# Kernel tuning notes

Measured on AMD Instinct MI355X. Metric: run time of the kernel, lower is better.

Reference implementation:

```python
import jax, jax.numpy as jnp
import numpy as np

HIDDEN_DIM = 2048
NUM_EXPERTS = 64
TOP_K = 2
NUM_TOKENS = 16384


def setup_inputs() -> dict:
    key = jax.random.key(0)
    kx, kw, kb = jax.random.split(key, 3)
    X = jax.random.normal(kx, (NUM_TOKENS, HIDDEN_DIM), dtype=jnp.float32)
    # nn.Linear(hidden_dim, num_experts): weight [num_experts, hidden_dim], bias [num_experts]
    bound = 1.0 / np.sqrt(HIDDEN_DIM)
    W = jax.random.uniform(kw, (NUM_EXPERTS, HIDDEN_DIM), minval=-bound, maxval=bound, dtype=jnp.float32)
    b = jax.random.uniform(kb, (NUM_EXPERTS,), minval=-bound, maxval=bound, dtype=jnp.float32)
    return {"X": X, "W": W, "b": b}


def reference(X, W, b):
    # router_logits = gate(X): [T, E]
    router_logits = jnp.einsum("th,eh->te", X, W) + b
    # softmax in float32 (matches dtype=torch.float)
    routing_probs = jax.nn.softmax(router_logits.astype(jnp.float32), axis=-1)
    # top-k over experts: [T, K]
    router_weights, selected_experts = jax.lax.top_k(routing_probs, TOP_K)
    # renormalize over selected experts (sum cast to X.dtype, result stays fp32 math)
    denom = jnp.sum(router_weights, axis=-1, keepdims=True).astype(X.dtype)
    router_weights = router_weights / denom
    # one-hot expert mask: [T, K, E], int64 like F.one_hot
    expert_mask = jax.nn.one_hot(selected_experts, NUM_EXPERTS, dtype=jnp.int32)
    return (router_logits, router_weights, selected_experts, expert_mask)
```

## Files before the change

kernel.cpp:

```cpp
#include <hip/hip_runtime.h>
#include <math.h>

constexpr int T_TOK = 16384;
constexpr int HDIM  = 2048;
constexpr int NEXP  = 64;
constexpr int TPB   = 64;
constexpr int NWAVE = 8;
constexpr int KPW   = HDIM / NWAVE;
constexpr int KSTEP = 32;
constexpr int NKS   = KPW / KSTEP;

typedef __attribute__((ext_vector_type(8))) short v8s;
typedef __attribute__((ext_vector_type(4))) float v4f;

#define MFMA_BF16 __builtin_amdgcn_mfma_f32_16x16x32_bf16

static __device__ __forceinline__ void split3(float x, unsigned short& h,
                                              unsigned short& m, unsigned short& l)
{
    unsigned u0 = __float_as_uint(x);
    h = (unsigned short)(u0 >> 16);
    float r1 = x - __uint_as_float(u0 & 0xFFFF0000u);
    unsigned u1 = __float_as_uint(r1);
    m = (unsigned short)(u1 >> 16);
    float r2 = r1 - __uint_as_float(u1 & 0xFFFF0000u);
    l = (unsigned short)(__float_as_uint(r2) >> 16);
}

static __device__ __forceinline__ void frag3(const float4& x0, const float4& x1,
                                             v8s& h, v8s& m, v8s& l)
{
    unsigned short sh, sm, sl;
    split3(x0.x, sh, sm, sl); h[0]=(short)sh; m[0]=(short)sm; l[0]=(short)sl;
    split3(x0.y, sh, sm, sl); h[1]=(short)sh; m[1]=(short)sm; l[1]=(short)sl;
    split3(x0.z, sh, sm, sl); h[2]=(short)sh; m[2]=(short)sm; l[2]=(short)sl;
    split3(x0.w, sh, sm, sl); h[3]=(short)sh; m[3]=(short)sm; l[3]=(short)sl;
    split3(x1.x, sh, sm, sl); h[4]=(short)sh; m[4]=(short)sm; l[4]=(short)sl;
    split3(x1.y, sh, sm, sl); h[5]=(short)sh; m[5]=(short)sm; l[5]=(short)sl;
    split3(x1.z, sh, sm, sl); h[6]=(short)sh; m[6]=(short)sm; l[6]=(short)sl;
    split3(x1.w, sh, sm, sl); h[7]=(short)sh; m[7]=(short)sm; l[7]=(short)sl;
}

static __device__ __forceinline__ int swz_e(int tok, int e) {
    return e ^ (((tok >> 2) & 1) << 4);
}

__global__ __launch_bounds__(512, 2)
void moe_router_mfma(const float* __restrict__ X,
                     const float* __restrict__ Wg,
                     const float* __restrict__ Bg,
                     float* __restrict__ out)
{
    __shared__ float red[4][TPB][NEXP];

    const int tid  = threadIdx.x;
    const int lane = tid & 63;
    const int wv   = tid >> 6;
    const int r16  = lane & 15;
    const int q    = lane >> 4;
    const int tok0 = blockIdx.x * TPB;

    const float* pA = X  + (size_t)(tok0 + r16) * HDIM + wv * KPW + q * 8;
    const float* pB = Wg + (size_t)r16 * HDIM + wv * KPW + q * 8;

    v4f acc[4][4];
#pragma unroll
    for (int mt = 0; mt < 4; ++mt)
#pragma unroll
        for (int nt = 0; nt < 4; ++nt)
            acc[mt][nt] = (v4f){0.f, 0.f, 0.f, 0.f};

    float4 a0[4], a1[4], b0[4], b1[4];
#pragma unroll
    for (int mt = 0; mt < 4; ++mt) {
        const float* p = pA + (size_t)mt * 16 * HDIM;
        a0[mt] = *(const float4*)p;
        a1[mt] = *(const float4*)(p + 4);
    }
#pragma unroll
    for (int nt = 0; nt < 4; ++nt) {
        const float* p = pB + (size_t)nt * 16 * HDIM;
        b0[nt] = *(const float4*)p;
        b1[nt] = *(const float4*)(p + 4);
    }

    for (int ks = 0; ks < NKS; ++ks) {
        v8s Ah[4], Am[4], Al[4], Bh[4], Bm[4], Bl[4];
#pragma unroll
        for (int mt = 0; mt < 4; ++mt) frag3(a0[mt], a1[mt], Ah[mt], Am[mt], Al[mt]);
#pragma unroll
        for (int nt = 0; nt < 4; ++nt) frag3(b0[nt], b1[nt], Bh[nt], Bm[nt], Bl[nt]);

        if (ks < NKS - 1) {
            const int off = (ks + 1) * KSTEP;
#pragma unroll
            for (int mt = 0; mt < 4; ++mt) {
                const float* p = pA + (size_t)mt * 16 * HDIM + off;
                a0[mt] = *(const float4*)p;
                a1[mt] = *(const float4*)(p + 4);
            }
#pragma unroll
            for (int nt = 0; nt < 4; ++nt) {
                const float* p = pB + (size_t)nt * 16 * HDIM + off;
                b0[nt] = *(const float4*)p;
                b1[nt] = *(const float4*)(p + 4);
            }
        }

#pragma unroll
        for (int mt = 0; mt < 4; ++mt)
#pragma unroll
            for (int nt = 0; nt < 4; ++nt) {
                v4f a = acc[mt][nt];
                a = MFMA_BF16(Ah[mt], Bh[nt], a, 0, 0, 0);
                a = MFMA_BF16(Ah[mt], Bm[nt], a, 0, 0, 0);
                a = MFMA_BF16(Am[mt], Bh[nt], a, 0, 0, 0);
                a = MFMA_BF16(Ah[mt], Bl[nt], a, 0, 0, 0);
                a = MFMA_BF16(Al[mt], Bh[nt], a, 0, 0, 0);
                a = MFMA_BF16(Am[mt], Bm[nt], a, 0, 0, 0);
                acc[mt][nt] = a;
            }
    }

    if (wv < 4) {
#pragma unroll
        for (int mt = 0; mt < 4; ++mt)
#pragma unroll
            for (int nt = 0; nt < 4; ++nt)
#pragma unroll
                for (int r = 0; r < 4; ++r) {
                    int tok = 16 * mt + q * 4 + r;
                    int e   = 16 * nt + r16;
                    red[wv][tok][swz_e(tok, e)] = acc[mt][nt][r];
                }
    }
    __syncthreads();
    if (wv >= 4) {
#pragma unroll
        for (int mt = 0; mt < 4; ++mt)
#pragma unroll
            for (int nt = 0; nt < 4; ++nt)
#pragma unroll
                for (int r = 0; r < 4; ++r) {
                    int tok = 16 * mt + q * 4 + r;
                    int e   = 16 * nt + r16;
                    red[wv - 4][tok][swz_e(tok, e)] += acc[mt][nt][r];
                }
    }
    __syncthreads();

    if (lane < 8) {
        const int tk = wv * 8 + lane;
        const int t  = tok0 + tk;
        float lg[NEXP];
#pragma unroll
        for (int e = 0; e < NEXP; ++e) {
            int es = swz_e(tk, e);
            lg[e] = ((red[0][tk][es] + red[1][tk][es]) +
                     (red[2][tk][es] + red[3][tk][es])) + Bg[e];
        }
        float* outL = out + (size_t)t * NEXP;
#pragma unroll
        for (int e = 0; e < NEXP; e += 4) {
            float4 v = make_float4(lg[e], lg[e+1], lg[e+2], lg[e+3]);
            *(float4*)(outL + e) = v;
        }
        float mx = lg[0];
#pragma unroll
        for (int e = 1; e < NEXP; ++e) mx = fmaxf(mx, lg[e]);
        float S = 0.f;
#pragma unroll
        for (int e = 0; e < NEXP; ++e) { lg[e] = expf(lg[e] - mx); S += lg[e]; }
#pragma unroll
        for (int e = 0; e < NEXP; ++e) lg[e] = lg[e] / S;

        float v1 = lg[0]; int i1 = 0;
        float v2 = -1.0f; int i2 = 0;
#pragma unroll
        for (int e = 1; e < NEXP; ++e) {
            float rv = lg[e];
            bool g1 = rv > v1;
            bool g2 = rv > v2;
            float nv2 = g1 ? v1 : (g2 ? rv : v2);
            int   ni2 = g1 ? i1 : (g2 ? e  : i2);
            v2 = nv2; i2 = ni2;
            v1 = g1 ? rv : v1;
            i1 = g1 ? e  : i1;
        }
        float den = v1 + v2;
        float w1 = v1 / den, w2 = v2 / den;

        float* outW = out + (size_t)T_TOK * NEXP;
        float* outS = outW + (size_t)T_TOK * 2;
        float* outM = outS + (size_t)T_TOK * 2;
        outW[2*t+0] = w1;        outW[2*t+1] = w2;
        outS[2*t+0] = (float)i1; outS[2*t+1] = (float)i2;

        float* mrow = outM + (size_t)t * 2 * NEXP;
#pragma unroll
        for (int e = 0; e < NEXP; e += 4) {
            float4 a = make_float4(e+0==i1?1.f:0.f, e+1==i1?1.f:0.f,
                                   e+2==i1?1.f:0.f, e+3==i1?1.f:0.f);
            *(float4*)(mrow + e) = a;
            float4 b = make_float4(e+0==i2?1.f:0.f, e+1==i2?1.f:0.f,
                                   e+2==i2?1.f:0.f, e+3==i2?1.f:0.f);
            *(float4*)(mrow + NEXP + e) = b;
        }
    }
}

extern "C" void kernel_launch(void* const* d_in, const int* in_sizes, int n_in,
                              void* d_out, int out_size, void* d_ws, size_t ws_size,
                              hipStream_t stream)
{
    const float* X = (const float*)d_in[0];
    const float* W = (const float*)d_in[1];
    const float* B = (const float*)d_in[2];
    float* out     = (float*)d_out;

    dim3 grid(T_TOK / TPB);
    dim3 block(512);
    hipLaunchKernelGGL(moe_router_mfma, grid, block, 0, stream, X, W, B, out);
}
```

Baseline: 222.3 us.

## Halve tokens per block to double grid size and raise occupancy

Cuts the token tile per block from 64 to 32, which doubles the grid and raises the launch-bounds occupancy hint from 2 to 4 blocks per CU. The goal is better latency hiding on a kernel that had only about one block per CU. The cost is that each block now re-reads and re-splits the gate weights over half as many tokens, so the conversion overhead per MFMA grows. The epilogue also rotates each lane's expert traversal order by lane*16 to spread shared-memory bank accesses, then maps the top-k indices back to real expert ids.

```diff
diff --git a/kernel.cpp b/kernel.cpp
--- a/kernel.cpp
+++ b/kernel.cpp
@@ -4,7 +4,8 @@
 constexpr int T_TOK = 16384;
 constexpr int HDIM  = 2048;
 constexpr int NEXP  = 64;
-constexpr int TPB   = 64;
+constexpr int TPB   = 32;
+constexpr int MT    = TPB / 16;
 constexpr int NWAVE = 8;
 constexpr int KPW   = HDIM / NWAVE;
 constexpr int KSTEP = 32;
@@ -45,7 +46,7 @@
     return e ^ (((tok >> 2) & 1) << 4);
 }
 
-__global__ __launch_bounds__(512, 2)
+__global__ __launch_bounds__(512, 4)
 void moe_router_mfma(const float* __restrict__ X,
                      const float* __restrict__ Wg,
                      const float* __restrict__ Bg,
@@ -63,16 +64,16 @@
     const float* pA = X  + (size_t)(tok0 + r16) * HDIM + wv * KPW + q * 8;
     const float* pB = Wg + (size_t)r16 * HDIM + wv * KPW + q * 8;
 
-    v4f acc[4][4];
-#pragma unroll
-    for (int mt = 0; mt < 4; ++mt)
+    v4f acc[MT][4];
+#pragma unroll
+    for (int mt = 0; mt < MT; ++mt)
 #pragma unroll
         for (int nt = 0; nt < 4; ++nt)
             acc[mt][nt] = (v4f){0.f, 0.f, 0.f, 0.f};
 
-    float4 a0[4], a1[4], b0[4], b1[4];
-#pragma unroll
-    for (int mt = 0; mt < 4; ++mt) {
+    float4 a0[MT], a1[MT], b0[4], b1[4];
+#pragma unroll
+    for (int mt = 0; mt < MT; ++mt) {
         const float* p = pA + (size_t)mt * 16 * HDIM;
         a0[mt] = *(const float4*)p;
         a1[mt] = *(const float4*)(p + 4);
@@ -85,16 +86,16 @@
     }
 
     for (int ks = 0; ks < NKS; ++ks) {
-        v8s Ah[4], Am[4], Al[4], Bh[4], Bm[4], Bl[4];
-#pragma unroll
-        for (int mt = 0; mt < 4; ++mt) frag3(a0[mt], a1[mt], Ah[mt], Am[mt], Al[mt]);
+        v8s Ah[MT], Am[MT], Al[MT], Bh[4], Bm[4], Bl[4];
+#pragma unroll
+        for (int mt = 0; mt < MT; ++mt) frag3(a0[mt], a1[mt], Ah[mt], Am[mt], Al[mt]);
 #pragma unroll
         for (int nt = 0; nt < 4; ++nt) frag3(b0[nt], b1[nt], Bh[nt], Bm[nt], Bl[nt]);
 
         if (ks < NKS - 1) {
             const int off = (ks + 1) * KSTEP;
 #pragma unroll
-            for (int mt = 0; mt < 4; ++mt) {
+            for (int mt = 0; mt < MT; ++mt) {
                 const float* p = pA + (size_t)mt * 16 * HDIM + off;
                 a0[mt] = *(const float4*)p;
                 a1[mt] = *(const float4*)(p + 4);
@@ -108,7 +109,7 @@
         }
 
 #pragma unroll
-        for (int mt = 0; mt < 4; ++mt)
+        for (int mt = 0; mt < MT; ++mt)
 #pragma unroll
             for (int nt = 0; nt < 4; ++nt) {
                 v4f a = acc[mt][nt];
@@ -124,7 +125,7 @@
 
     if (wv < 4) {
 #pragma unroll
-        for (int mt = 0; mt < 4; ++mt)
+        for (int mt = 0; mt < MT; ++mt)
 #pragma unroll
             for (int nt = 0; nt < 4; ++nt)
 #pragma unroll
@@ -137,7 +138,7 @@
     __syncthreads();
     if (wv >= 4) {
 #pragma unroll
-        for (int mt = 0; mt < 4; ++mt)
+        for (int mt = 0; mt < MT; ++mt)
 #pragma unroll
             for (int nt = 0; nt < 4; ++nt)
 #pragma unroll
@@ -149,44 +150,49 @@
     }
     __syncthreads();
 
-    if (lane < 8) {
-        const int tk = wv * 8 + lane;
+    if (lane < 4) {
+        const int tk = wv * 4 + lane;
         const int t  = tok0 + tk;
+        const int sh = lane << 4;
         float lg[NEXP];
 #pragma unroll
-        for (int e = 0; e < NEXP; ++e) {
+        for (int eo = 0; eo < NEXP; ++eo) {
+            int e  = (eo + sh) & (NEXP - 1);
             int es = swz_e(tk, e);
-            lg[e] = ((red[0][tk][es] + red[1][tk][es]) +
-                     (red[2][tk][es] + red[3][tk][es])) + Bg[e];
+            lg[eo] = ((red[0][tk][es] + red[1][tk][es]) +
+                      (red[2][tk][es] + red[3][tk][es])) + Bg[e];
         }
         float* outL = out + (size_t)t * NEXP;
 #pragma unroll
-        for (int e = 0; e < NEXP; e += 4) {
-            float4 v = make_float4(lg[e], lg[e+1], lg[e+2], lg[e+3]);
+        for (int eo = 0; eo < NEXP; eo += 4) {
+            int e = (eo + sh) & (NEXP - 1);
+            float4 v = make_float4(lg[eo], lg[eo+1], lg[eo+2], lg[eo+3]);
             *(float4*)(outL + e) = v;
         }
         float mx = lg[0];
 #pragma unroll
-        for (int e = 1; e < NEXP; ++e) mx = fmaxf(mx, lg[e]);
+        for (int eo = 1; eo < NEXP; ++eo) mx = fmaxf(mx, lg[eo]);
         float S = 0.f;
 #pragma unroll
-        for (int e = 0; e < NEXP; ++e) { lg[e] = expf(lg[e] - mx); S += lg[e]; }
-#pragma unroll
-        for (int e = 0; e < NEXP; ++e) lg[e] = lg[e] / S;
-
-        float v1 = lg[0]; int i1 = 0;
-        float v2 = -1.0f; int i2 = 0;
-#pragma unroll
-        for (int e = 1; e < NEXP; ++e) {
-            float rv = lg[e];
+        for (int eo = 0; eo < NEXP; ++eo) { lg[eo] = expf(lg[eo] - mx); S += lg[eo]; }
+#pragma unroll
+        for (int eo = 0; eo < NEXP; ++eo) lg[eo] = lg[eo] / S;
+
+        float v1 = lg[0]; int i1o = 0;
+        float v2 = -1.0f; int i2o = 0;
+#pragma unroll
+        for (int eo = 1; eo < NEXP; ++eo) {
+            float rv = lg[eo];
             bool g1 = rv > v1;
             bool g2 = rv > v2;
             float nv2 = g1 ? v1 : (g2 ? rv : v2);
-            int   ni2 = g1 ? i1 : (g2 ? e  : i2);
-            v2 = nv2; i2 = ni2;
+            int   ni2 = g1 ? i1o : (g2 ? eo : i2o);
+            v2 = nv2; i2o = ni2;
             v1 = g1 ? rv : v1;
-            i1 = g1 ? e  : i1;
-        }
+            i1o = g1 ? eo : i1o;
+        }
+        const int i1 = (i1o + sh) & (NEXP - 1);
+        const int i2 = (i2o + sh) & (NEXP - 1);
         float den = v1 + v2;
         float w1 = v1 / den, w2 = v2 / den;
 
```

After: 263.2 us. +18.4%, slower.

## Prepack W into bf16 split fragments and stage X through swizzled LDS

Applied to the files above, without the earlier changes.

A small pre-kernel splits W into hi/mid/lo bf16 MFMA fragments once, laid out for coalesced per-lane loads, so the main kernel no longer re-splits W for every token block. The X tile is loaded coalesced by row into a double-buffered, XOR-swizzled shared-memory region per wave and then read back in MFMA fragment order. The K loop is fully unrolled with register prefetch of both operands. Costs are an extra kernel launch, workspace use, 128KB of LDS (which can lower occupancy below the launch bound of 2 blocks), and higher register pressure from prefetching 12 B fragments.

```diff
diff --git a/kernel.cpp b/kernel.cpp
--- a/kernel.cpp
+++ b/kernel.cpp
@@ -5,6 +5,7 @@
 constexpr int HDIM  = 2048;
 constexpr int NEXP  = 64;
 constexpr int TPB   = 64;
+constexpr int MT    = TPB / 16;
 constexpr int NWAVE = 8;
 constexpr int KPW   = HDIM / NWAVE;
 constexpr int KSTEP = 32;
@@ -45,13 +46,33 @@
     return e ^ (((tok >> 2) & 1) << 4);
 }
 
+__global__ __launch_bounds__(256)
+void pack_w_kernel(const float* __restrict__ W, short* __restrict__ P)
+{
+    const int tid = blockIdx.x * 256 + threadIdx.x;
+    const int l   = tid & 63;
+    int g = tid >> 6;
+    const int p  = g % 3;  g /= 3;
+    const int nt = g % 4;  g /= 4;
+    const int ks = g % 8;
+    const int wv = g / 8;
+    const int r16 = l & 15, q = l >> 4;
+    const float* src = W + (size_t)(nt * 16 + r16) * HDIM + wv * KPW + ks * KSTEP + q * 8;
+    float4 x0 = *(const float4*)src;
+    float4 x1 = *(const float4*)(src + 4);
+    v8s h, m, lo;
+    frag3(x0, x1, h, m, lo);
+    v8s outv = (p == 0) ? h : (p == 1) ? m : lo;
+    *(v8s*)(P + (size_t)tid * 8) = outv;
+}
+
 __global__ __launch_bounds__(512, 2)
 void moe_router_mfma(const float* __restrict__ X,
-                     const float* __restrict__ Wg,
+                     const short* __restrict__ Pw,
                      const float* __restrict__ Bg,
                      float* __restrict__ out)
 {
-    __shared__ float red[4][TPB][NEXP];
+    __shared__ float smem[32768];
 
     const int tid  = threadIdx.x;
     const int lane = tid & 63;
@@ -60,71 +81,90 @@
     const int q    = lane >> 4;
     const int tok0 = blockIdx.x * TPB;
 
-    const float* pA = X  + (size_t)(tok0 + r16) * HDIM + wv * KPW + q * 8;
-    const float* pB = Wg + (size_t)r16 * HDIM + wv * KPW + q * 8;
-
-    v4f acc[4][4];
-#pragma unroll
-    for (int mt = 0; mt < 4; ++mt)
+    const int wrow = lane >> 3;
+    const int lc   = lane & 7;
+    const int sc   = (lc ^ wrow) * 4;
+    const float* pS = X + (size_t)(tok0 + wrow) * HDIM + wv * KPW + lc * 4;
+
+    const int xsl = wv * 4096;
+    const int rc0 = ((2 * q)     ^ (r16 & 7)) * 4;
+    const int rc1 = ((2 * q + 1) ^ (r16 & 7)) * 4;
+
+    const short* pBw = Pw + (size_t)(wv * 8) * 12 * 512 + lane * 8;
+
+    v4f acc[MT][4];
+#pragma unroll
+    for (int mt = 0; mt < MT; ++mt)
 #pragma unroll
         for (int nt = 0; nt < 4; ++nt)
             acc[mt][nt] = (v4f){0.f, 0.f, 0.f, 0.f};
 
-    float4 a0[4], a1[4], b0[4], b1[4];
-#pragma unroll
-    for (int mt = 0; mt < 4; ++mt) {
-        const float* p = pA + (size_t)mt * 16 * HDIM;
-        a0[mt] = *(const float4*)p;
-        a1[mt] = *(const float4*)(p + 4);
-    }
-#pragma unroll
-    for (int nt = 0; nt < 4; ++nt) {
-        const float* p = pB + (size_t)nt * 16 * HDIM;
-        b0[nt] = *(const float4*)p;
-        b1[nt] = *(const float4*)(p + 4);
-    }
-
+#pragma unroll
+    for (int j = 0; j < 8; ++j) {
+        float4 gv = *(const float4*)(pS + (size_t)j * 8 * HDIM);
+        *(float4*)&smem[xsl + (j * 8 + wrow) * 32 + sc] = gv;
+    }
+    v8s Bc[12];
+#pragma unroll
+    for (int c = 0; c < 12; ++c) Bc[c] = *(const v8s*)(pBw + c * 512);
+
+#pragma unroll
     for (int ks = 0; ks < NKS; ++ks) {
-        v8s Ah[4], Am[4], Al[4], Bh[4], Bm[4], Bl[4];
-#pragma unroll
-        for (int mt = 0; mt < 4; ++mt) frag3(a0[mt], a1[mt], Ah[mt], Am[mt], Al[mt]);
-#pragma unroll
-        for (int nt = 0; nt < 4; ++nt) frag3(b0[nt], b1[nt], Bh[nt], Bm[nt], Bl[nt]);
-
+        const int cur = xsl + (ks & 1) * 2048;
+        const int nxt = xsl + ((ks + 1) & 1) * 2048;
+
+        float4 g[8];
         if (ks < NKS - 1) {
-            const int off = (ks + 1) * KSTEP;
-#pragma unroll
-            for (int mt = 0; mt < 4; ++mt) {
-                const float* p = pA + (size_t)mt * 16 * HDIM + off;
-                a0[mt] = *(const float4*)p;
-                a1[mt] = *(const float4*)(p + 4);
-            }
-#pragma unroll
-            for (int nt = 0; nt < 4; ++nt) {
-                const float* p = pB + (size_t)nt * 16 * HDIM + off;
-                b0[nt] = *(const float4*)p;
-                b1[nt] = *(const float4*)(p + 4);
-            }
-        }
-
-#pragma unroll
-        for (int mt = 0; mt < 4; ++mt)
+#pragma unroll
+            for (int j = 0; j < 8; ++j)
+                g[j] = *(const float4*)(pS + (size_t)j * 8 * HDIM + (ks + 1) * KSTEP);
+        }
+
+        v8s Bn[12];
+        if (ks < NKS - 1) {
+            const short* pBk = pBw + (ks + 1) * 6144;
+#pragma unroll
+            for (int c = 0; c < 12; ++c) Bn[c] = *(const v8s*)(pBk + c * 512);
+        }
+
+        float4 a0[MT], a1[MT];
+#pragma unroll
+        for (int mt = 0; mt < MT; ++mt) {
+            const int rowb = cur + (16 * mt + r16) * 32;
+            a0[mt] = *(const float4*)&smem[rowb + rc0];
+            a1[mt] = *(const float4*)&smem[rowb + rc1];
+        }
+
+#pragma unroll
+        for (int mt = 0; mt < MT; ++mt) {
+            v8s Ah, Am, Al;
+            frag3(a0[mt], a1[mt], Ah, Am, Al);
 #pragma unroll
             for (int nt = 0; nt < 4; ++nt) {
                 v4f a = acc[mt][nt];
-                a = MFMA_BF16(Ah[mt], Bh[nt], a, 0, 0, 0);
-                a = MFMA_BF16(Ah[mt], Bm[nt], a, 0, 0, 0);
-                a = MFMA_BF16(Am[mt], Bh[nt], a, 0, 0, 0);
-                a = MFMA_BF16(Ah[mt], Bl[nt], a, 0, 0, 0);
-                a = MFMA_BF16(Al[mt], Bh[nt], a, 0, 0, 0);
-                a = MFMA_BF16(Am[mt], Bm[nt], a, 0, 0, 0);
+                a = MFMA_BF16(Ah, Bc[nt * 3 + 0], a, 0, 0, 0);
+                a = MFMA_BF16(Ah, Bc[nt * 3 + 1], a, 0, 0, 0);
+                a = MFMA_BF16(Am, Bc[nt * 3 + 0], a, 0, 0, 0);
+                a = MFMA_BF16(Ah, Bc[nt * 3 + 2], a, 0, 0, 0);
+                a = MFMA_BF16(Al, Bc[nt * 3 + 0], a, 0, 0, 0);
+                a = MFMA_BF16(Am, Bc[nt * 3 + 1], a, 0, 0, 0);
                 acc[mt][nt] = a;
             }
-    }
-
+        }
+
+        if (ks < NKS - 1) {
+#pragma unroll
+            for (int j = 0; j < 8; ++j)
+                *(float4*)&smem[nxt + (j * 8 + wrow) * 32 + sc] = g[j];
+#pragma unroll
+            for (int c = 0; c < 12; ++c) Bc[c] = Bn[c];
+        }
+    }
+
+    float (*red)[TPB][NEXP] = (float (*)[TPB][NEXP])smem;
     if (wv < 4) {
 #pragma unroll
-        for (int mt = 0; mt < 4; ++mt)
+        for (int mt = 0; mt < MT; ++mt)
 #pragma unroll
             for (int nt = 0; nt < 4; ++nt)
 #pragma unroll
@@ -137,7 +177,7 @@
     __syncthreads();
     if (wv >= 4) {
 #pragma unroll
-        for (int mt = 0; mt < 4; ++mt)
+        for (int mt = 0; mt < MT; ++mt)
 #pragma unroll
             for (int nt = 0; nt < 4; ++nt)
 #pragma unroll
@@ -218,7 +258,10 @@
     const float* B = (const float*)d_in[2];
     float* out     = (float*)d_out;
 
-    dim3 grid(T_TOK / TPB);
-    dim3 block(512);
-    hipLaunchKernelGGL(moe_router_mfma, grid, block, 0, stream, X, W, B, out);
-}
+    short* Pw = (short*)d_ws;
+
+    hipLaunchKernelGGL(pack_w_kernel, dim3(49152 / 256), dim3(256),
+                       0, stream, W, Pw);
+    hipLaunchKernelGGL(moe_router_mfma, dim3(T_TOK / TPB), dim3(512),
+                       0, stream, X, Pw, B, out);
+}
```

After: 228.7 us. 2.9% more time.
